# Kernel optimization log

Measured on AMD Instinct MI355X. Metric: run time of the kernel, lower is better.

## Reference

```python
import jax, jax.numpy as jnp
import numpy as np

DIM = 768
HEADS = 12
DIM_HEAD = 64
INNER = HEADS * DIM_HEAD
L = 256
EPS = 1e-08


def setup_inputs() -> dict:
    key = jax.random.key(0)
    k1, k2, k3, k4 = jax.random.split(key, 4)
    x = jax.random.normal(k1, (2, 4096, DIM), dtype=jnp.float32)
    # Linear weights stored torch-style: (out_features, in_features)
    w_qkv = jax.random.normal(k2, (3 * INNER, DIM), dtype=jnp.float32) * (DIM ** -0.5)
    w_out = jax.random.normal(k3, (DIM, INNER), dtype=jnp.float32) * (INNER ** -0.5)
    b_out = jax.random.normal(k4, (DIM,), dtype=jnp.float32) * 0.01
    # learned per-head log-scale temperature, init log2(L^2 - L)
    scale = jnp.full((HEADS,), np.log2(L * L - L), dtype=jnp.float32)
    return {"x": x, "w_qkv": w_qkv, "w_out": w_out, "b_out": b_out, "scale": scale}


def reference(x, w_qkv, w_out, b_out, scale):
    b, n, d = x.shape
    h, dh = HEADS, DIM_HEAD
    qkv = x @ w_qkv.T                                   # [b, n, 3*inner]
    q, k, v = jnp.split(qkv, 3, axis=-1)
    # [b, n, h, dh] -> [b, h, n, dh]
    q, k, v = (t.reshape(b, n, h, dh).transpose(0, 2, 1, 3) for t in (q, k, v))
    # Faithful to source: L2 norm over the HEADS axis (dim=1), then rsqrt
    q = q * jax.lax.rsqrt(jnp.linalg.norm(q, axis=1, keepdims=True) + EPS)
    k = k * jax.lax.rsqrt(jnp.linalg.norm(k, axis=1, keepdims=True) + EPS)
    dots = jnp.einsum('bhid,bhjd->bhij', q, k)          # [b, h, n, n]
    scores = jax.nn.softmax(dots / scale[:, None, None], axis=-1)
    out = jnp.einsum('bhij,bhjd->bhid', scores, v)      # [b, h, n, dh]
    out = out.transpose(0, 2, 1, 3).reshape(b, n, h * dh)
    return out @ w_out.T + b_out
```

## Files before the change

kernel.cpp:

```cpp
#include <hip/hip_runtime.h>
#include <hip/hip_bf16.h>

#define DIMX   768
#define HEADS  12
#define DH     64
#define INNER  768
#define NQKV   2304
#define SEQ    4096
#define BATCH  2
#define ROWS   (BATCH*SEQ)
#define EPSF   1e-8f
#define LOG2E  1.4426950408889634f

typedef __bf16 bf16x8 __attribute__((ext_vector_type(8)));
typedef float  f32x4  __attribute__((ext_vector_type(4)));
typedef float  f32x16 __attribute__((ext_vector_type(16)));

__device__ __forceinline__ unsigned short f2bf(float f) {
    unsigned int u = __float_as_uint(f);
    unsigned int r = ((u >> 16) & 1u) + 0x7FFFu;
    return (unsigned short)((u + r) >> 16);
}
__device__ __forceinline__ float bf2f(unsigned short u) {
    return __builtin_bit_cast(float, (unsigned)u << 16);
}
__device__ __forceinline__ unsigned pkbf(float a, float b) {
    unsigned short la = __builtin_bit_cast(unsigned short, (__bf16)a);
    unsigned short lb = __builtin_bit_cast(unsigned short, (__bf16)b);
    return (unsigned)la | ((unsigned)lb << 16);
}

__global__ __launch_bounds__(256) void cast_f32_bf16(
    const float* __restrict__ src, unsigned short* __restrict__ dst, int n)
{
    int i = (blockIdx.x * 256 + threadIdx.x) * 4;
    if (i + 3 < n) {
        float4 v = *reinterpret_cast<const float4*>(src + i);
        ushort4 o;
        o.x = f2bf(v.x); o.y = f2bf(v.y); o.z = f2bf(v.z); o.w = f2bf(v.w);
        *reinterpret_cast<ushort4*>(dst + i) = o;
    }
}

template<bool BF16OUT>
__global__ __launch_bounds__(256) void gemm_bt_kernel(
    const unsigned short* __restrict__ A,
    const unsigned short* __restrict__ B,
    void* __restrict__ Cv,
    const float* __restrict__ bias,
    int M, int N, int K)
{
    __shared__ unsigned short shA[128][72];
    __shared__ unsigned short shB[128][72];

    const int bm0 = blockIdx.x * 128;
    const int bn0 = blockIdx.y * 128;
    const int tid = threadIdx.x;
    const int lane = tid & 63;
    const int wid  = tid >> 6;
    const int l15  = lane & 15;
    const int l4   = lane >> 4;
    const int wr   = wid >> 1;
    const int wc   = wid & 1;

    f32x4 acc[4][4];
    #pragma unroll
    for (int i = 0; i < 4; ++i)
        #pragma unroll
        for (int j = 0; j < 4; ++j)
            acc[i][j] = (f32x4){0.f, 0.f, 0.f, 0.f};

    const int nkt = K >> 6;
    for (int kt = 0; kt < nkt; ++kt) {
        const int k0 = kt << 6;
        __syncthreads();
        #pragma unroll
        for (int it = 0; it < 4; ++it) {
            int c = tid + it * 256;
            int row = c >> 3, colc = c & 7;
            *reinterpret_cast<uint4*>(&shA[row][colc * 8]) =
                *reinterpret_cast<const uint4*>(&A[(size_t)(bm0 + row) * K + k0 + colc * 8]);
            *reinterpret_cast<uint4*>(&shB[row][colc * 8]) =
                *reinterpret_cast<const uint4*>(&B[(size_t)(bn0 + row) * K + k0 + colc * 8]);
        }
        __syncthreads();
        #pragma unroll
        for (int ks = 0; ks < 2; ++ks) {
            bf16x8 af[4], bfr[4];
            #pragma unroll
            for (int mf = 0; mf < 4; ++mf)
                af[mf] = *reinterpret_cast<const bf16x8*>(&shA[wr * 64 + mf * 16 + l15][ks * 32 + l4 * 8]);
            #pragma unroll
            for (int nf = 0; nf < 4; ++nf)
                bfr[nf] = *reinterpret_cast<const bf16x8*>(&shB[wc * 64 + nf * 16 + l15][ks * 32 + l4 * 8]);
            #pragma unroll
            for (int mf = 0; mf < 4; ++mf)
                #pragma unroll
                for (int nf = 0; nf < 4; ++nf)
                    acc[mf][nf] = __builtin_amdgcn_mfma_f32_16x16x32_bf16(
                        af[mf], bfr[nf], acc[mf][nf], 0, 0, 0);
        }
    }

    #pragma unroll
    for (int mf = 0; mf < 4; ++mf) {
        #pragma unroll
        for (int nf = 0; nf < 4; ++nf) {
            int col = bn0 + wc * 64 + nf * 16 + l15;
            float badd = bias ? bias[col] : 0.f;
            #pragma unroll
            for (int r = 0; r < 4; ++r) {
                int row = bm0 + wr * 64 + mf * 16 + l4 * 4 + r;
                if constexpr (BF16OUT)
                    ((unsigned short*)Cv)[(size_t)row * N + col] = f2bf(acc[mf][nf][r] + badd);
                else
                    ((float*)Cv)[(size_t)row * N + col] = acc[mf][nf][r] + badd;
            }
        }
    }
}

__global__ __launch_bounds__(256) void normalize_kernel(
    const unsigned short* __restrict__ qkv,
    const float* __restrict__ scale,
    unsigned short* __restrict__ qo,
    unsigned short* __restrict__ ko)
{
    int t = blockIdx.x * 256 + threadIdx.x;
    int row = t >> 6;
    int d = t & 63;
    int b = row >> 12;
    int n = row & 4095;
    const unsigned short* base = qkv + (size_t)row * NQKV;

    float qv[12], kv[12];
    float sq = 0.f, sk = 0.f;
    #pragma unroll
    for (int h = 0; h < 12; ++h) {
        qv[h] = bf2f(base[h * 64 + d]);
        kv[h] = bf2f(base[768 + h * 64 + d]);
        sq += qv[h] * qv[h];
        sk += kv[h] * kv[h];
    }
    float rq = rsqrtf(sqrtf(sq) + EPSF);
    float rk = rsqrtf(sqrtf(sk) + EPSF);
    #pragma unroll
    for (int h = 0; h < 12; ++h) {
        size_t bh = (size_t)(b * 12 + h);
        float fold = LOG2E / scale[h];
        qo[(bh * SEQ + n) * 64 + d] = f2bf(qv[h] * rq * fold);
        ko[(bh * SEQ + n) * 64 + d] = f2bf(kv[h] * rk);
    }
}

__global__ __launch_bounds__(256) void vtrans_kernel(
    const unsigned short* __restrict__ qkv,
    unsigned short* __restrict__ vt)
{
    __shared__ unsigned short tile[64][72];
    const int bh = blockIdx.x;
    const int nt = blockIdx.y;
    const int b = bh / HEADS, h = bh % HEADS;
    const int tid = threadIdx.x;

    #pragma unroll
    for (int it = 0; it < 2; ++it) {
        int c = tid + it * 256;
        int r = c >> 3, cc = c & 7;
        *reinterpret_cast<uint4*>(&tile[r][cc * 8]) =
            *reinterpret_cast<const uint4*>(
                &qkv[(size_t)(b * SEQ + nt * 64 + r) * NQKV + 1536 + h * 64 + cc * 8]);
    }
    __syncthreads();
    #pragma unroll
    for (int it = 0; it < 2; ++it) {
        int c = tid + it * 256;
        int d = c >> 3, nc = c & 7;
        ushort4 o0, o1;
        o0.x = tile[nc * 8 + 0][d]; o0.y = tile[nc * 8 + 1][d];
        o0.z = tile[nc * 8 + 2][d]; o0.w = tile[nc * 8 + 3][d];
        o1.x = tile[nc * 8 + 4][d]; o1.y = tile[nc * 8 + 5][d];
        o1.z = tile[nc * 8 + 6][d]; o1.w = tile[nc * 8 + 7][d];
        unsigned short* dst = &vt[((size_t)bh * 64 + d) * SEQ + nt * 64 + nc * 8];
        *reinterpret_cast<ushort4*>(dst)     = o0;
        *reinterpret_cast<ushort4*>(dst + 4) = o1;
    }
}

__global__ __launch_bounds__(256) void attn_kernel(
    const unsigned short* __restrict__ qg,
    const unsigned short* __restrict__ kg,
    const unsigned short* __restrict__ vtg,
    unsigned short* __restrict__ attnout)
{
    __shared__ unsigned short shK[64][72];
    __shared__ unsigned short shV[64][72];

    const int qblk = blockIdx.x;
    const int bh   = blockIdx.y;
    const int b    = bh / HEADS;
    const int h    = bh % HEADS;
    const int tid  = threadIdx.x;
    const int lane = tid & 63;
    const int wid  = tid >> 6;
    const int l31  = lane & 31;
    const int hi   = lane >> 5;

    bf16x8 qf[4];
    {
        const unsigned short* qrow =
            qg + ((size_t)bh * SEQ + qblk * 128 + wid * 32 + l31) * 64 + hi * 8;
        #pragma unroll
        for (int d0 = 0; d0 < 4; ++d0)
            qf[d0] = *reinterpret_cast<const bf16x8*>(qrow + d0 * 16);
    }

    f32x16 ot[2];
    #pragma unroll
    for (int r = 0; r < 16; ++r) { ot[0][r] = 0.f; ot[1][r] = 0.f; }
    float l_lane = 0.f;

    const unsigned short* kbase = kg  + (size_t)bh * SEQ * 64;
    const unsigned short* vbase = vtg + (size_t)bh * 64 * SEQ;

    for (int kt = 0; kt < SEQ / 64; ++kt) {
        __syncthreads();
        #pragma unroll
        for (int it = 0; it < 2; ++it) {
            int c = tid + it * 256;
            int row = c >> 3, colc = c & 7;
            *reinterpret_cast<uint4*>(&shK[row][colc * 8]) =
                *reinterpret_cast<const uint4*>(&kbase[(size_t)(kt * 64 + row) * 64 + colc * 8]);
            *reinterpret_cast<uint4*>(&shV[row][colc * 8]) =
                *reinterpret_cast<const uint4*>(&vbase[(size_t)row * SEQ + kt * 64 + colc * 8]);
        }
        __syncthreads();

        f32x16 st0, st1;
        #pragma unroll
        for (int r = 0; r < 16; ++r) { st0[r] = 0.f; st1[r] = 0.f; }
        #pragma unroll
        for (int d0 = 0; d0 < 4; ++d0) {
            bf16x8 kf0 = *reinterpret_cast<const bf16x8*>(&shK[l31][d0 * 16 + hi * 8]);
            bf16x8 kf1 = *reinterpret_cast<const bf16x8*>(&shK[32 + l31][d0 * 16 + hi * 8]);
            st0 = __builtin_amdgcn_mfma_f32_32x32x16_bf16(kf0, qf[d0], st0, 0, 0, 0);
            st1 = __builtin_amdgcn_mfma_f32_32x32x16_bf16(kf1, qf[d0], st1, 0, 0, 0);
        }

        float s0 = 0.f, s1 = 0.f, s2 = 0.f, s3 = 0.f;
        unsigned cp0[8], cp1[8];
        #pragma unroll
        for (int t = 0; t < 8; ++t) {
            float pa = __builtin_amdgcn_exp2f(st0[2 * t]);
            float pb = __builtin_amdgcn_exp2f(st0[2 * t + 1]);
            float pc = __builtin_amdgcn_exp2f(st1[2 * t]);
            float pd = __builtin_amdgcn_exp2f(st1[2 * t + 1]);
            s0 += pa; s1 += pb; s2 += pc; s3 += pd;
            cp0[t] = pkbf(pa, pb);
            cp1[t] = pkbf(pc, pd);
        }
        l_lane += (s0 + s1) + (s2 + s3);

        #pragma unroll
        for (int cb = 0; cb < 2; ++cb) {
            #pragma unroll
            for (int kk = 0; kk < 2; ++kk) {
                unsigned c0 = cb ? cp1[4 * kk + 0] : cp0[4 * kk + 0];
                unsigned c1 = cb ? cp1[4 * kk + 1] : cp0[4 * kk + 1];
                unsigned c2 = cb ? cp1[4 * kk + 2] : cp0[4 * kk + 2];
                unsigned c3 = cb ? cp1[4 * kk + 3] : cp0[4 * kk + 3];
                unsigned e0 = __shfl_xor(c0, 32);
                unsigned e1 = __shfl_xor(c1, 32);
                unsigned e2 = __shfl_xor(c2, 32);
                unsigned e3 = __shfl_xor(c3, 32);
                union { unsigned uu[4]; bf16x8 v; } pu;
                pu.uu[0] = hi ? e2 : c0;
                pu.uu[1] = hi ? e3 : c1;
                pu.uu[2] = hi ? c2 : e0;
                pu.uu[3] = hi ? c3 : e1;
                #pragma unroll
                for (int df = 0; df < 2; ++df) {
                    bf16x8 vf = *reinterpret_cast<const bf16x8*>(
                        &shV[df * 32 + l31][cb * 32 + kk * 16 + hi * 8]);
                    ot[df] = __builtin_amdgcn_mfma_f32_32x32x16_bf16(vf, pu.v, ot[df], 0, 0, 0);
                }
            }
        }
    }

    float l_all = l_lane + __shfl_xor(l_lane, 32);
    float invl = 1.0f / l_all;
    int n = qblk * 128 + wid * 32 + l31;
    unsigned short* orow = attnout + ((size_t)(b * SEQ + n)) * INNER + h * 64;
    #pragma unroll
    for (int df = 0; df < 2; ++df) {
        #pragma unroll
        for (int t = 0; t < 4; ++t) {
            unsigned w0 = pkbf(ot[df][4 * t]     * invl, ot[df][4 * t + 1] * invl);
            unsigned w1 = pkbf(ot[df][4 * t + 2] * invl, ot[df][4 * t + 3] * invl);
            unsigned long long pk = (unsigned long long)w0 | ((unsigned long long)w1 << 32);
            *reinterpret_cast<unsigned long long*>(orow + df * 32 + t * 8 + hi * 4) = pk;
        }
    }
}

extern "C" void kernel_launch(void* const* d_in, const int* in_sizes, int n_in,
                              void* d_out, int out_size, void* d_ws, size_t ws_size,
                              hipStream_t stream)
{
    const float* x      = (const float*)d_in[0];
    const float* w_qkv  = (const float*)d_in[1];
    const float* w_out  = (const float*)d_in[2];
    const float* b_out  = (const float*)d_in[3];
    const float* scale  = (const float*)d_in[4];
    float* out = (float*)d_out;
    char* ws = (char*)d_ws;

    unsigned short* xb    = (unsigned short*)(ws);
    unsigned short* wqkvb = (unsigned short*)(ws + 12582912);
    unsigned short* woutb = (unsigned short*)(ws + 16121856);
    unsigned short* attnb = (unsigned short*)(ws + 17301504);
    unsigned short* qb    = (unsigned short*)(ws + 29884416);
    unsigned short* kb    = (unsigned short*)(ws + 42467328);
    unsigned short* vtb   = (unsigned short*)(ws + 55050240);
    unsigned short* qkvb  = (unsigned short*)(ws + 67633152);

    cast_f32_bf16<<<6144, 256, 0, stream>>>(x, xb, 6291456);
    cast_f32_bf16<<<1728, 256, 0, stream>>>(w_qkv, wqkvb, 1769472);
    cast_f32_bf16<<<576, 256, 0, stream>>>(w_out, woutb, 589824);

    gemm_bt_kernel<true><<<dim3(64, 18), 256, 0, stream>>>(xb, wqkvb, qkvb, nullptr, ROWS, NQKV, DIMX);

    normalize_kernel<<<2048, 256, 0, stream>>>(qkvb, scale, qb, kb);
    vtrans_kernel<<<dim3(BATCH * HEADS, SEQ / 64), 256, 0, stream>>>(qkvb, vtb);

    attn_kernel<<<dim3(SEQ / 128, BATCH * HEADS), 256, 0, stream>>>(qb, kb, vtb, attnb);

    gemm_bt_kernel<false><<<dim3(64, 6), 256, 0, stream>>>(attnb, woutb, out, b_out, ROWS, INNER, INNER);
}
```

Before: 254.0 us.

## Use direct global-to-LDS loads, XCD-aware attention grid, and permlane32 swaps

The GEMM tile loads now use global_load_lds to write straight into unpadded shared memory, so tiles no longer pass through registers. The attention grid is flattened and remapped so each XCD handles three whole (batch, head) pairs, improving L2 reuse of K/V. The cross-half-wave exchange of P fragments uses permlane32_swap instead of four shuffles plus selects. Dropping the row padding may add LDS bank conflicts on the MFMA fragment reads.

```diff
diff --git a/kernel.cpp b/kernel.cpp
--- a/kernel.cpp
+++ b/kernel.cpp
@@ -15,6 +15,7 @@
 typedef __bf16 bf16x8 __attribute__((ext_vector_type(8)));
 typedef float  f32x4  __attribute__((ext_vector_type(4)));
 typedef float  f32x16 __attribute__((ext_vector_type(16)));
+typedef unsigned u32x2 __attribute__((ext_vector_type(2)));
 
 __device__ __forceinline__ unsigned short f2bf(float f) {
     unsigned int u = __float_as_uint(f);
@@ -28,6 +29,12 @@
     unsigned short la = __builtin_bit_cast(unsigned short, (__bf16)a);
     unsigned short lb = __builtin_bit_cast(unsigned short, (__bf16)b);
     return (unsigned)la | ((unsigned)lb << 16);
+}
+
+__device__ __forceinline__ void gload_lds16(const void* g, void* l) {
+    __builtin_amdgcn_global_load_lds(
+        (const __attribute__((address_space(1))) void*)g,
+        (__attribute__((address_space(3))) void*)l, 16, 0, 0);
 }
 
 __global__ __launch_bounds__(256) void cast_f32_bf16(
@@ -50,8 +57,8 @@
     const float* __restrict__ bias,
     int M, int N, int K)
 {
-    __shared__ unsigned short shA[128][72];
-    __shared__ unsigned short shB[128][72];
+    __shared__ unsigned short shA[128][64];
+    __shared__ unsigned short shB[128][64];
 
     const int bm0 = blockIdx.x * 128;
     const int bn0 = blockIdx.y * 128;
@@ -62,6 +69,8 @@
     const int l4   = lane >> 4;
     const int wr   = wid >> 1;
     const int wc   = wid & 1;
+    const int srow = lane >> 3;
+    const int scol = (lane & 7) * 8;
 
     f32x4 acc[4][4];
     #pragma unroll
@@ -75,13 +84,10 @@
         const int k0 = kt << 6;
         __syncthreads();
         #pragma unroll
-        for (int it = 0; it < 4; ++it) {
-            int c = tid + it * 256;
-            int row = c >> 3, colc = c & 7;
-            *reinterpret_cast<uint4*>(&shA[row][colc * 8]) =
-                *reinterpret_cast<const uint4*>(&A[(size_t)(bm0 + row) * K + k0 + colc * 8]);
-            *reinterpret_cast<uint4*>(&shB[row][colc * 8]) =
-                *reinterpret_cast<const uint4*>(&B[(size_t)(bn0 + row) * K + k0 + colc * 8]);
+        for (int j = 0; j < 4; ++j) {
+            int row = wid * 32 + j * 8;
+            gload_lds16(&A[(size_t)(bm0 + row + srow) * K + k0 + scol], &shA[row][0]);
+            gload_lds16(&B[(size_t)(bn0 + row + srow) * K + k0 + scol], &shB[row][0]);
         }
         __syncthreads();
         #pragma unroll
@@ -196,10 +202,14 @@
     __shared__ unsigned short shK[64][72];
     __shared__ unsigned short shV[64][72];
 
-    const int qblk = blockIdx.x;
-    const int bh   = blockIdx.y;
+    const int wg   = blockIdx.x;
+    const int xcd  = wg & 7;
+    const int slot = wg >> 3;
+    const int bh   = xcd * 3 + (slot >> 5);
+    const int qblk = slot & 31;
     const int b    = bh / HEADS;
     const int h    = bh % HEADS;
+
     const int tid  = threadIdx.x;
     const int lane = tid & 63;
     const int wid  = tid >> 6;
@@ -269,15 +279,13 @@
                 unsigned c1 = cb ? cp1[4 * kk + 1] : cp0[4 * kk + 1];
                 unsigned c2 = cb ? cp1[4 * kk + 2] : cp0[4 * kk + 2];
                 unsigned c3 = cb ? cp1[4 * kk + 3] : cp0[4 * kk + 3];
-                unsigned e0 = __shfl_xor(c0, 32);
-                unsigned e1 = __shfl_xor(c1, 32);
-                unsigned e2 = __shfl_xor(c2, 32);
-                unsigned e3 = __shfl_xor(c3, 32);
+                u32x2 s = __builtin_amdgcn_permlane32_swap(c0, c2, false, false);
+                u32x2 t = __builtin_amdgcn_permlane32_swap(c1, c3, false, false);
                 union { unsigned uu[4]; bf16x8 v; } pu;
-                pu.uu[0] = hi ? e2 : c0;
-                pu.uu[1] = hi ? e3 : c1;
-                pu.uu[2] = hi ? c2 : e0;
-                pu.uu[3] = hi ? c3 : e1;
+                pu.uu[0] = s.x;
+                pu.uu[1] = t.x;
+                pu.uu[2] = s.y;
+                pu.uu[3] = t.y;
                 #pragma unroll
                 for (int df = 0; df < 2; ++df) {
                     bf16x8 vf = *reinterpret_cast<const bf16x8*>(
@@ -334,7 +342,7 @@
     normalize_kernel<<<2048, 256, 0, stream>>>(qkvb, scale, qb, kb);
     vtrans_kernel<<<dim3(BATCH * HEADS, SEQ / 64), 256, 0, stream>>>(qkvb, vtb);
 
-    attn_kernel<<<dim3(SEQ / 128, BATCH * HEADS), 256, 0, stream>>>(qb, kb, vtb, attnb);
+    attn_kernel<<<768, 256, 0, stream>>>(qb, kb, vtb, attnb);
 
     gemm_bt_kernel<false><<<dim3(64, 6), 256, 0, stream>>>(attnb, woutb, out, b_out, ROWS, INNER, INNER);
 }
```

Measured after the change: 255.5 us. Within noise of the previous version (+0.6%).
